# Kernel optimization log

Hardware: AMD Instinct MI355X
Metric: run time of the kernel (lower is better)

Reference implementation:

```python
import jax, jax.numpy as jnp
import numpy as np

B, T1, T2, D = 4, 128, 128, 300


def setup_inputs() -> dict:
    key = jax.random.key(0)
    ks = jax.random.split(key, 9)
    s = 1.0 / np.sqrt(D)
    return {
        "query": jax.random.normal(ks[0], (B, T1, D), jnp.float32),
        "key": jax.random.normal(ks[1], (B, T2, D), jnp.float32),
        "value": jax.random.normal(ks[2], (B, T2, D), jnp.float32),
        "hL": jax.random.normal(ks[3], (B, T1, T2, D), jnp.float32),
        "hR": jax.random.normal(ks[4], (B, T2, T1, D), jnp.float32),
        "WQ": jax.random.uniform(ks[5], (D, D), jnp.float32, -s, s),
        "bQ": jax.random.uniform(ks[6], (D,), jnp.float32, -s, s),
        "WK": jax.random.uniform(ks[7], (D, D), jnp.float32, -s, s),
        "bK": jax.random.uniform(ks[8], (D,), jnp.float32, -s, s),
    }


def reference(query, key, value, hL, hR, WQ, bQ, WK, bK):
    # Linear projections (torch nn.Linear: x @ W.T + b). Note fwK is applied
    # to BOTH key and value in the original module.
    q = query @ WQ.T + bQ            # [B, T1, D]
    k = key @ WK.T + bK              # [B, T2, D]
    v = value @ WK.T + bK            # [B, T2, D]

    hR_t = jnp.swapaxes(hR, 1, 2)    # [B, T1, T2, D]

    # concept-augmented scores: (q_i + hL_ij) . (k_j + hR_ji)
    q_plus_hL = q[:, :, None, :] + hL          # [B, T1, T2, D]
    k_plus_hR = k[:, None, :, :] + hR_t        # [B, T1, T2, D]
    scores = jnp.einsum("bijd,bijd->bij", q_plus_hL, k_plus_hR)  # [B, T1, T2]

    p_attn = jax.nn.softmax(scores, axis=-1)   # [B, T1, T2] (dropout p=0.0)

    # sharpening=True path: re-softmax with temperature 1/1000 then clamp
    attn = jnp.clip(jax.nn.softmax(1000.0 * p_attn, axis=-1), 0.0, 1.0)

    v_aug = v[:, None, :, :] + hR_t            # [B, T1, T2, D]
    x = jnp.einsum("bij,bijd->bid", attn, v_aug)  # [B, T1, D]
    return x
```

## Files before the change

### kernel.cpp

```cpp
#include <hip/hip_runtime.h>

#define BB 4
#define T 128
#define D 300
#define D4 75
#define NROW 512

__global__ __launch_bounds__(320) void proj_kernel(
    const float* __restrict__ query, const float* __restrict__ key,
    const float* __restrict__ value,
    const float* __restrict__ WQ, const float* __restrict__ bQ,
    const float* __restrict__ WK, const float* __restrict__ bK,
    float* __restrict__ qkv )
{
    const int src  = blockIdx.x >> 6;
    const int rblk = blockIdx.x & 63;
    const int r0   = rblk * 8;
    const float* in   = (src == 0) ? query : (src == 1 ? key : value);
    const float* W    = (src == 0) ? WQ : WK;
    const float* bias = (src == 0) ? bQ : bK;
    float* out = qkv + src * (NROW * D);

    __shared__ __align__(16) float lds_in[8 * D];
    for (int idx = threadIdx.x; idx < 8 * D; idx += 320)
        lds_in[idx] = in[r0 * D + idx];
    __syncthreads();

    const int t = threadIdx.x;
    if (t < D) {
        float acc[8];
        const float bv = bias[t];
        #pragma unroll
        for (int r = 0; r < 8; ++r) acc[r] = bv;
        const float4* W4 = (const float4*)(W + t * D);
        for (int e4 = 0; e4 < D4; ++e4) {
            const float4 w = W4[e4];
            #pragma unroll
            for (int r = 0; r < 8; ++r) {
                const float4 x = *(const float4*)(&lds_in[r * D + e4 * 4]);
                acc[r] += w.x * x.x + w.y * x.y + w.z * x.z + w.w * x.w;
            }
        }
        #pragma unroll
        for (int r = 0; r < 8; ++r)
            out[(r0 + r) * D + t] = acc[r];
    }
}

__global__ __launch_bounds__(256) void score_kernel(
    const float* __restrict__ hL, const float* __restrict__ hR,
    const float* __restrict__ qkv, float* __restrict__ S)
{
    const int b  = blockIdx.x >> 10;
    const int it = (blockIdx.x >> 5) & 31;
    const int jt = blockIdx.x & 31;
    const int i0 = it * 4, j0 = jt * 4;

    __shared__ __align__(16) float4 lds[2400];

    const float4* hL4 = (const float4*)hL;
    const float4* hR4 = (const float4*)hR;

    for (int f = threadIdx.x; f < 2400; f += 256) {
        if (f < 1200) {
            const int run = f / 300;
            const int t   = f - run * 300;
            lds[f] = hL4[(size_t)((b * T + i0 + run) * T + j0) * D4 + t];
        } else {
            const int g   = f - 1200;
            const int run = g / 300;
            const int t   = g - run * 300;
            lds[f] = hR4[(size_t)((b * T + j0 + run) * T + i0) * D4 + t];
        }
    }
    __syncthreads();

    const int w    = threadIdx.x >> 6;
    const int lane = threadIdx.x & 63;

    const float4* q4     = (const float4*)(qkv) + (size_t)(b * T + i0 + w) * D4;
    const float4* kbase4 = (const float4*)(qkv + NROW * D);

    const float4 qa = q4[lane];
    float4 qb = {0.f, 0.f, 0.f, 0.f};
    if (lane < D4 - 64) qb = q4[64 + lane];

    #pragma unroll
    for (int jl = 0; jl < 4; ++jl) {
        const float4* k4 = kbase4 + (size_t)(b * T + j0 + jl) * D4;
        const float4 ka = k4[lane];
        const float4 la = lds[w * 300 + jl * 75 + lane];
        const float4 ra = lds[1200 + jl * 300 + w * 75 + lane];
        float s = (qa.x + la.x) * (ka.x + ra.x) + (qa.y + la.y) * (ka.y + ra.y)
                + (qa.z + la.z) * (ka.z + ra.z) + (qa.w + la.w) * (ka.w + ra.w);
        if (lane < D4 - 64) {
            const float4 kb = k4[64 + lane];
            const float4 lb = lds[w * 300 + jl * 75 + 64 + lane];
            const float4 rb = lds[1200 + jl * 300 + w * 75 + 64 + lane];
            s += (qb.x + lb.x) * (kb.x + rb.x) + (qb.y + lb.y) * (kb.y + rb.y)
               + (qb.z + lb.z) * (kb.z + rb.z) + (qb.w + lb.w) * (kb.w + rb.w);
        }
        #pragma unroll
        for (int off = 32; off > 0; off >>= 1)
            s += __shfl_down(s, off, 64);
        if (lane == 0)
            S[(size_t)(b * T + i0 + w) * T + j0 + jl] = s;
    }
}

__global__ __launch_bounds__(320) void out_kernel(
    const float* __restrict__ S, const float* __restrict__ qkv,
    const float* __restrict__ hR, float* __restrict__ outp)
{
    const int b = blockIdx.x >> 7;
    const int i = blockIdx.x & 127;
    __shared__ float sc[T];
    const int tid = threadIdx.x;

    if (tid < 64) {
        const float* Srow = S + (size_t)(b * T + i) * T;
        float s0 = Srow[tid], s1 = Srow[tid + 64];
        float m = fmaxf(s0, s1);
        #pragma unroll
        for (int off = 32; off > 0; off >>= 1) m = fmaxf(m, __shfl_xor(m, off, 64));
        float e0 = __expf(s0 - m), e1 = __expf(s1 - m);
        float sum = e0 + e1;
        #pragma unroll
        for (int off = 32; off > 0; off >>= 1) sum += __shfl_xor(sum, off, 64);
        const float inv = 1.0f / sum;
        float t0 = 1000.0f * (e0 * inv), t1 = 1000.0f * (e1 * inv);
        float m2 = fmaxf(t0, t1);
        #pragma unroll
        for (int off = 32; off > 0; off >>= 1) m2 = fmaxf(m2, __shfl_xor(m2, off, 64));
        float f0 = __expf(t0 - m2), f1 = __expf(t1 - m2);
        float sum2 = f0 + f1;
        #pragma unroll
        for (int off = 32; off > 0; off >>= 1) sum2 += __shfl_xor(sum2, off, 64);
        const float inv2 = 1.0f / sum2;
        sc[tid]      = fminf(fmaxf(f0 * inv2, 0.f), 1.f);
        sc[tid + 64] = fminf(fmaxf(f1 * inv2, 0.f), 1.f);
    }
    __syncthreads();

    if (tid < D) {
        float acc = 0.f;
        const float* vb = qkv + 2 * NROW * D + b * T * D;
        for (int j = 0; j < T; ++j) {
            const float aj = sc[j];
            if (aj >= 1e-12f)
                acc += aj * (vb[j * D + tid] + hR[((size_t)(b * T + j) * T + i) * D + tid]);
        }
        outp[(size_t)(b * T + i) * D + tid] = acc;
    }
}

extern "C" void kernel_launch(void* const* d_in, const int* in_sizes, int n_in,
                              void* d_out, int out_size, void* d_ws, size_t ws_size,
                              hipStream_t stream) {
    const float* query = (const float*)d_in[0];
    const float* key   = (const float*)d_in[1];
    const float* value = (const float*)d_in[2];
    const float* hL    = (const float*)d_in[3];
    const float* hR    = (const float*)d_in[4];
    const float* WQ    = (const float*)d_in[5];
    const float* bQ    = (const float*)d_in[6];
    const float* WK    = (const float*)d_in[7];
    const float* bK    = (const float*)d_in[8];
    float* out = (float*)d_out;
    float* qkv = (float*)d_ws;
    float* S   = qkv + 3 * NROW * D;

    proj_kernel<<<dim3(192), dim3(320), 0, stream>>>(query, key, value, WQ, bQ, WK, bK, qkv);
    score_kernel<<<dim3(4096), dim3(256), 0, stream>>>(hL, hR, qkv, S);
    out_kernel<<<dim3(512), dim3(320), 0, stream>>>(S, qkv, hR, out);
}
```

Before: 239.9 us.

## Stream hL/hR directly from global in score kernel, drop LDS staging

The score kernel no longer stages hL/hR tiles in shared memory. Each wavefront now computes 16 scores for one row, loading hL, hR and k straight from global memory with four j-values in flight per batch, and writes four scores at once with a float4 store. The grid shrinks to 1024 blocks with a launch-bounds occupancy hint. This removes the LDS round trip and the block-wide barrier in exchange for more live registers and scattered hR reads, which are strided by T*D.

```diff
diff --git a/kernel.cpp b/kernel.cpp
--- a/kernel.cpp
+++ b/kernel.cpp
@@ -1,4 +1,5 @@
 #include <hip/hip_runtime.h>
+#include <stdint.h>
 
 #define BB 4
 #define T 128
@@ -47,64 +48,68 @@
     }
 }
 
-__global__ __launch_bounds__(256) void score_kernel(
+__global__ __launch_bounds__(256, 4) void score_kernel(
     const float* __restrict__ hL, const float* __restrict__ hR,
     const float* __restrict__ qkv, float* __restrict__ S)
 {
-    const int b  = blockIdx.x >> 10;
-    const int it = (blockIdx.x >> 5) & 31;
-    const int jt = blockIdx.x & 31;
-    const int i0 = it * 4, j0 = jt * 4;
-
-    __shared__ __align__(16) float4 lds[2400];
+    const int gtid = blockIdx.x * 256 + threadIdx.x;
+    const int wv   = gtid >> 6;
+    const int lane = gtid & 63;
+    const int row  = wv >> 3;
+    const int seg  = wv & 7;
+    const int b    = row >> 7;
+    const int i    = row & 127;
+    const int j0   = seg * 16;
 
     const float4* hL4 = (const float4*)hL;
     const float4* hR4 = (const float4*)hR;
+    const float4* q4  = (const float4*)qkv + (size_t)row * D4;
+    const float4* k4b = (const float4*)qkv + (size_t)NROW * D4 + (size_t)b * T * D4;
 
-    for (int f = threadIdx.x; f < 2400; f += 256) {
-        if (f < 1200) {
-            const int run = f / 300;
-            const int t   = f - run * 300;
-            lds[f] = hL4[(size_t)((b * T + i0 + run) * T + j0) * D4 + t];
-        } else {
-            const int g   = f - 1200;
-            const int run = g / 300;
-            const int t   = g - run * 300;
-            lds[f] = hR4[(size_t)((b * T + j0 + run) * T + i0) * D4 + t];
-        }
-    }
-    __syncthreads();
-
-    const int w    = threadIdx.x >> 6;
-    const int lane = threadIdx.x & 63;
-
-    const float4* q4     = (const float4*)(qkv) + (size_t)(b * T + i0 + w) * D4;
-    const float4* kbase4 = (const float4*)(qkv + NROW * D);
-
+    const bool tail = lane < (D4 - 64);
+    const float4 zz = make_float4(0.f, 0.f, 0.f, 0.f);
     const float4 qa = q4[lane];
-    float4 qb = {0.f, 0.f, 0.f, 0.f};
-    if (lane < D4 - 64) qb = q4[64 + lane];
+    const float4 qb = tail ? q4[64 + lane] : zz;
 
     #pragma unroll
-    for (int jl = 0; jl < 4; ++jl) {
-        const float4* k4 = kbase4 + (size_t)(b * T + j0 + jl) * D4;
-        const float4 ka = k4[lane];
-        const float4 la = lds[w * 300 + jl * 75 + lane];
-        const float4 ra = lds[1200 + jl * 300 + w * 75 + lane];
-        float s = (qa.x + la.x) * (ka.x + ra.x) + (qa.y + la.y) * (ka.y + ra.y)
-                + (qa.z + la.z) * (ka.z + ra.z) + (qa.w + la.w) * (ka.w + ra.w);
-        if (lane < D4 - 64) {
-            const float4 kb = k4[64 + lane];
-            const float4 lb = lds[w * 300 + jl * 75 + 64 + lane];
-            const float4 rb = lds[1200 + jl * 300 + w * 75 + 64 + lane];
-            s += (qb.x + lb.x) * (kb.x + rb.x) + (qb.y + lb.y) * (kb.y + rb.y)
-               + (qb.z + lb.z) * (kb.z + rb.z) + (qb.w + lb.w) * (kb.w + rb.w);
+    for (int m = 0; m < 4; ++m) {
+        const int j = j0 + m * 4;
+        float4 lA[4], lB[4], rA[4], rB[4], kA[4], kB[4];
+        #pragma unroll
+        for (int u = 0; u < 4; ++u) {
+            const size_t pL = ((size_t)row * T + (j + u)) * D4;
+            const size_t pR = ((size_t)(b * T + j + u) * T + i) * D4;
+            const size_t pK = (size_t)(j + u) * D4;
+            lA[u] = hL4[pL + lane];
+            rA[u] = hR4[pR + lane];
+            kA[u] = k4b[pK + lane];
+            lB[u] = tail ? hL4[pL + 64 + lane] : zz;
+            rB[u] = tail ? hR4[pR + 64 + lane] : zz;
+            kB[u] = tail ? k4b[pK + 64 + lane] : zz;
+        }
+        float4 s;
+        float* sp = &s.x;
+        #pragma unroll
+        for (int u = 0; u < 4; ++u) {
+            float v = (qa.x + lA[u].x) * (kA[u].x + rA[u].x)
+                    + (qa.y + lA[u].y) * (kA[u].y + rA[u].y)
+                    + (qa.z + lA[u].z) * (kA[u].z + rA[u].z)
+                    + (qa.w + lA[u].w) * (kA[u].w + rA[u].w);
+            v += (qb.x + lB[u].x) * (kB[u].x + rB[u].x)
+               + (qb.y + lB[u].y) * (kB[u].y + rB[u].y)
+               + (qb.z + lB[u].z) * (kB[u].z + rB[u].z)
+               + (qb.w + lB[u].w) * (kB[u].w + rB[u].w);
+            sp[u] = v;
         }
         #pragma unroll
-        for (int off = 32; off > 0; off >>= 1)
-            s += __shfl_down(s, off, 64);
+        for (int off = 32; off > 0; off >>= 1) {
+            s.x += __shfl_xor(s.x, off, 64);
+            s.y += __shfl_xor(s.y, off, 64);
+            s.z += __shfl_xor(s.z, off, 64);
+            s.w += __shfl_xor(s.w, off, 64);
+        }
         if (lane == 0)
-            S[(size_t)(b * T + i0 + w) * T + j0 + jl] = s;
+            *(float4*)&S[(size_t)row * T + j] = s;
     }
 }
 
@@ -171,6 +176,6 @@
     float* S   = qkv + 3 * NROW * D;
 
     proj_kernel<<<dim3(192), dim3(320), 0, stream>>>(query, key, value, WQ, bQ, WK, bK, qkv);
-    score_kernel<<<dim3(4096), dim3(256), 0, stream>>>(hL, hR, qkv, S);
+    score_kernel<<<dim3(1024), dim3(256), 0, stream>>>(hL, hR, qkv, S);
     out_kernel<<<dim3(512), dim3(320), 0, stream>>>(S, qkv, hR, out);
 }
```

New measurement: 258.1 us. 1.08x slower.
